# Kernel tuning notes

Measured on AMD Instinct MI355X. Metric: run time of the kernel, lower is better.

## Reference

```python
import jax, jax.numpy as jnp
import numpy as np

# Faithful JAX translation of fastmax_function with mask=True, p=1, normalize=0.
# In that branch the torch code sets temperature = 1 and uses a0 = a1 = 1.

def setup_inputs() -> dict:
    key = jax.random.key(0)
    kq, kk, kv = jax.random.split(key, 3)
    b, h, n, d = 2, 8, 8192, 32
    q = jax.random.normal(kq, (b, h, n, d), dtype=jnp.float32)
    k = jax.random.normal(kk, (b, h, n, d), dtype=jnp.float32)
    v = jax.random.normal(kv, (b, h, n, d), dtype=jnp.float32)
    return {"q": q, "k": k, "v": v}


def reference(q, k, v):
    # q, k, v: (b, h, n, d); causal (mask=True), p=1, a0=a1=1, temperature=1
    b, h, n, d = q.shape
    # first term: running sum of values
    first = jnp.cumsum(v, axis=2)                                  # (b,h,n,d)
    # second term: q_i . (sum_{j<=i} k_j v_j^T)
    kv = jnp.einsum('bhnd,bhne->bhnde', k, v)                      # (b,h,n,d,d)
    kv_cs = jnp.cumsum(kv, axis=2)                                 # (b,h,n,d,d)
    second = jnp.einsum('bhnd,bhnde->bhne', q, kv_cs)              # (b,h,n,d)
    # denominator: i + q_i . (sum_{j<=i} k_j)
    k_cs = jnp.cumsum(k, axis=2)                                   # (b,h,n,d)
    div1 = jnp.arange(1, n + 1, dtype=q.dtype)                     # (n,)
    div2 = jnp.einsum('bhnd,bhnd->bhn', q, k_cs)                   # (b,h,n)
    div = (div1[None, None, :] + div2)[..., None]                  # (b,h,n,1)
    return (first + second) / div
```

## Files before the change

### kernel.cpp

```cpp
#include <hip/hip_runtime.h>


#define D      32
#define C      64
#define NCHUNK 128
#define GSIZE  8
#define NGROUP 16
#define BH     16
#define NBLK   (BH * NCHUNK)
#define STATE  1088

typedef __attribute__((ext_vector_type(8))) short bf16x8;
typedef __attribute__((ext_vector_type(4))) float f32x4;
typedef __attribute__((ext_vector_type(4))) unsigned short u16x4;

__device__ __forceinline__ unsigned short f2bf(float x) {
  union { float f; unsigned u; } c; c.f = x;
  unsigned r = (c.u + 0x7FFFu + ((c.u >> 16) & 1u)) >> 16;
  return (unsigned short)r;
}

__device__ __forceinline__ int permcol(int e) {
  return (e & 1) ? (16 + (e >> 1)) : (e >> 1);
}

__device__ __forceinline__ float4 add4(float4 a, float4 b) {
  return make_float4(a.x + b.x, a.y + b.y, a.z + b.z, a.w + b.w);
}

__global__ __launch_bounds__(256) void state_scan_kernel(
    const float* __restrict__ k, const float* __restrict__ v,
    float* __restrict__ states, float* __restrict__ totals) {
  int blk = blockIdx.x;
  int c0  = blk * GSIZE;
  const float4* kp = (const float4*)k + (size_t)c0 * 512;
  const float4* vp = (const float4*)v + (size_t)c0 * 512;

  __shared__ __align__(16) unsigned short kT[D * 72];
  __shared__ __align__(16) unsigned short vT[D * 72];
  __shared__ __align__(16) float4 psK[256];
  __shared__ __align__(16) float4 psV[256];

  int t  = threadIdx.x;
  int j0 = t >> 3;
  int cb = (t & 7) * 4;
  int lane = t & 63, w = t >> 6;
  int m16 = lane & 15, quad = lane >> 4;
  int mb = w >> 1, nb = w & 1;
  int d1b = 16 * mb + quad * 4;
  int d2  = 16 * nb + m16;

  float pref[4] = {0.f, 0.f, 0.f, 0.f};
  float tailpref = 0.f;

  float4 kA = kp[t], kB = kp[t + 256];
  float4 vA = vp[t], vB = vp[t + 256];

  for (int ci = 0; ci < GSIZE; ++ci) {
    {
      const float* ka = &kA.x; const float* kb = &kB.x;
      const float* va = &vA.x; const float* vb = &vB.x;
#pragma unroll
      for (int cc = 0; cc < 4; ++cc) {
        kT[(cb + cc) * 72 + j0]      = f2bf(ka[cc]);
        kT[(cb + cc) * 72 + j0 + 32] = f2bf(kb[cc]);
        vT[(cb + cc) * 72 + j0]      = f2bf(va[cc]);
        vT[(cb + cc) * 72 + j0 + 32] = f2bf(vb[cc]);
      }
      psK[t] = make_float4(kA.x + kB.x, kA.y + kB.y, kA.z + kB.z, kA.w + kB.w);
      psV[t] = make_float4(vA.x + vB.x, vA.y + vB.y, vA.z + vB.z, vA.w + vB.w);
    }
    __syncthreads();

    if (ci + 1 < GSIZE) {
      const float4* kn = kp + (size_t)(ci + 1) * 512;
      const float4* vn = vp + (size_t)(ci + 1) * 512;
      kA = kn[t]; kB = kn[t + 256];
      vA = vn[t]; vB = vn[t + 256];
    }

    f32x4 acc = {0.f, 0.f, 0.f, 0.f};
#pragma unroll
    for (int kb2 = 0; kb2 < 2; ++kb2) {
      bf16x8 a = *(const bf16x8*)&kT[(16 * mb + m16) * 72 + kb2 * 32 + quad * 8];
      bf16x8 b = *(const bf16x8*)&vT[(16 * nb + m16) * 72 + kb2 * 32 + quad * 8];
      acc = __builtin_amdgcn_mfma_f32_16x16x32_bf16(a, b, acc, 0, 0, 0);
    }
    float csum = 0.f;
    if (t < 64) {
      int ee = t & 31;
      const float* ps = (t < 32) ? (const float*)psK : (const float*)psV;
#pragma unroll
      for (int m = 0; m < 32; ++m) csum += ps[ee + 32 * m];
    }

    float* stC = states + (size_t)(c0 + ci) * STATE;
#pragma unroll
    for (int reg = 0; reg < 4; ++reg) {
      stC[(d1b + reg) * 32 + d2] = pref[reg];
      pref[reg] += acc[reg];
    }
    if (t < 64) {
      stC[1024 + t] = tailpref;
      tailpref += csum;
    }
    __syncthreads();
  }

  float* tp = totals + (size_t)blk * STATE;
#pragma unroll
  for (int reg = 0; reg < 4; ++reg) tp[(d1b + reg) * 32 + d2] = pref[reg];
  if (t < 64) tp[1024 + t] = tailpref;
}

__global__ __launch_bounds__(256) void output_kernel(
    const float* __restrict__ q, const float* __restrict__ k,
    const float* __restrict__ v, const float* __restrict__ states,
    const float* __restrict__ totals, float* __restrict__ out) {
  int blk = blockIdx.x;
  int c   = blk & 127;
  int bh  = blk >> 7;
  int g   = c >> 3;
  size_t off = (size_t)blk * (C * D);
  const float4* qp4 = (const float4*)q + (size_t)blk * 512;
  const float4* kp4 = (const float4*)k + (size_t)blk * 512;
  const float4* vp4 = (const float4*)v + (size_t)blk * 512;
  const float4* st4 = (const float4*)(states + (size_t)blk * STATE);
  const float4* tb4 = (const float4*)(totals + (size_t)(bh * NGROUP) * STATE);

  __shared__ __align__(16) unsigned short qbf[C * 40];
  __shared__ __align__(16) unsigned short kbf[C * 40];
  __shared__ __align__(16) unsigned short vTbf[D * 72];
  __shared__ __align__(16) unsigned short kvTbf[D * 40];
  __shared__ __align__(16) unsigned short Tbf[C * 72];
  __shared__ __align__(16) float q_s[C * 36];
  __shared__ __align__(16) float kc_s[C * 36];
  __shared__ __align__(16) float gtot[8 * 32];
  __shared__ __align__(16) float kpre_s[D], vpre_s[D], invdiv_s[C];

  int t  = threadIdx.x;
  int j0 = t >> 3;
  int cb = (t & 7) * 4;

  float4 qA = qp4[t], qB = qp4[t + 256];
  float4 kA = kp4[t], kB = kp4[t + 256];
  float4 vA = vp4[t], vB = vp4[t + 256];
  float4 sv = st4[t];
  float4 tail = make_float4(0.f, 0.f, 0.f, 0.f);
  if (t < 16) tail = st4[256 + t];

  {
    float4 a0 = make_float4(0.f, 0.f, 0.f, 0.f), a1 = a0, a2 = a0, a3 = a0;
    int gp = 0;
    for (; gp + 4 <= g; gp += 4) {
      a0 = add4(a0, tb4[(size_t)(gp + 0) * 272 + t]);
      a1 = add4(a1, tb4[(size_t)(gp + 1) * 272 + t]);
      a2 = add4(a2, tb4[(size_t)(gp + 2) * 272 + t]);
      a3 = add4(a3, tb4[(size_t)(gp + 3) * 272 + t]);
    }
    for (; gp < g; ++gp) a0 = add4(a0, tb4[(size_t)gp * 272 + t]);
    sv = add4(sv, add4(add4(a0, a1), add4(a2, a3)));
    if (t < 16)
      for (int g2 = 0; g2 < g; ++g2)
        tail = add4(tail, tb4[(size_t)g2 * 272 + 256 + t]);
  }

  for (int z = t; z < (C * 72) / 8; z += 256)
    ((uint4*)Tbf)[z] = make_uint4(0, 0, 0, 0);

  *(float4*)&q_s[j0 * 36 + cb]         = qA;
  *(float4*)&q_s[(j0 + 32) * 36 + cb]  = qB;
  *(float4*)&kc_s[j0 * 36 + cb]        = kA;
  *(float4*)&kc_s[(j0 + 32) * 36 + cb] = kB;
  *(u16x4*)&qbf[j0 * 40 + cb] =
      (u16x4){f2bf(qA.x), f2bf(qA.y), f2bf(qA.z), f2bf(qA.w)};
  *(u16x4*)&qbf[(j0 + 32) * 40 + cb] =
      (u16x4){f2bf(qB.x), f2bf(qB.y), f2bf(qB.z), f2bf(qB.w)};
  *(u16x4*)&kbf[j0 * 40 + cb] =
      (u16x4){f2bf(kA.x), f2bf(kA.y), f2bf(kA.z), f2bf(kA.w)};
  *(u16x4*)&kbf[(j0 + 32) * 40 + cb] =
      (u16x4){f2bf(kB.x), f2bf(kB.y), f2bf(kB.z), f2bf(kB.w)};
  {
    const float* va = &vA.x; const float* vb = &vB.x;
    const float* sp = &sv.x;
#pragma unroll
    for (int cc = 0; cc < 4; ++cc) {
      int n = permcol(cb + cc);
      vTbf[n * 72 + j0]      = f2bf(va[cc]);
      vTbf[n * 72 + j0 + 32] = f2bf(vb[cc]);
      kvTbf[n * 40 + j0]     = f2bf(sp[cc]);
    }
  }
  if (t < 8)            ((float4*)kpre_s)[t]     = tail;
  else if (t < 16)      ((float4*)vpre_s)[t - 8] = tail;
  __syncthreads();

  int lane = t & 63, w = t >> 6;
  int m16 = lane & 15, quad = lane >> 4;

  const bf16x8 aQ = *(const bf16x8*)&qbf[(16 * w + m16) * 40 + quad * 8];
  for (int jb = 0; jb <= w; ++jb) {
    bf16x8 bK = *(const bf16x8*)&kbf[(16 * jb + m16) * 40 + quad * 8];
    f32x4 cS = {0.f, 0.f, 0.f, 0.f};
    cS = __builtin_amdgcn_mfma_f32_16x16x32_bf16(aQ, bK, cS, 0, 0, 0);
    int jcol = 16 * jb + m16;
#pragma unroll
    for (int reg = 0; reg < 4; ++reg) {
      int i = 16 * w + quad * 4 + reg;
      float tv = (jcol <= i) ? (1.f + cS[reg]) : 0.f;
      Tbf[i * 72 + jcol] = f2bf(tv);
    }
  }
  int rg = t >> 5;
  int e  = t & 31;
  float vals[8];
  {
    float run = 0.f;
#pragma unroll
    for (int r = 0; r < 8; ++r) {
      vals[r] = kc_s[(rg * 8 + r) * 36 + e];
      run += vals[r];
    }
    gtot[rg * 32 + e] = run;
  }
  __syncthreads();

  {
    float offv = kpre_s[e];
    for (int g2 = 0; g2 < rg; ++g2) offv += gtot[g2 * 32 + e];
    float cacc = offv;
#pragma unroll
    for (int r = 0; r < 8; ++r) {
      cacc += vals[r];
      kc_s[(rg * 8 + r) * 36 + e] = cacc;
    }
  }
  __syncthreads();

  if (t < 64) {
    int i = t;
    float dp = 0.f;
#pragma unroll
    for (int d4 = 0; d4 < 8; ++d4) {
      float4 qv = *(const float4*)&q_s[i * 36 + 4 * d4];
      float4 kc = *(const float4*)&kc_s[i * 36 + 4 * d4];
      dp += qv.x * kc.x + qv.y * kc.y + qv.z * kc.z + qv.w * kc.w;
    }
    invdiv_s[i] = 1.f / ((float)(c * C + i + 1) + dp);
  }
  f32x4 o0 = {0.f, 0.f, 0.f, 0.f}, o1 = {0.f, 0.f, 0.f, 0.f};
  {
    bf16x8 b0 = *(const bf16x8*)&kvTbf[(m16)      * 40 + quad * 8];
    bf16x8 b1 = *(const bf16x8*)&kvTbf[(16 + m16) * 40 + quad * 8];
    o0 = __builtin_amdgcn_mfma_f32_16x16x32_bf16(aQ, b0, o0, 0, 0, 0);
    o1 = __builtin_amdgcn_mfma_f32_16x16x32_bf16(aQ, b1, o1, 0, 0, 0);
  }
  int kbcnt = (w >= 2) ? 2 : 1;
  for (int kb2 = 0; kb2 < kbcnt; ++kb2) {
    bf16x8 aT = *(const bf16x8*)&Tbf[(16 * w + m16) * 72 + kb2 * 32 + quad * 8];
    bf16x8 b0 = *(const bf16x8*)&vTbf[(m16)      * 72 + kb2 * 32 + quad * 8];
    bf16x8 b1 = *(const bf16x8*)&vTbf[(16 + m16) * 72 + kb2 * 32 + quad * 8];
    o0 = __builtin_amdgcn_mfma_f32_16x16x32_bf16(aT, b0, o0, 0, 0, 0);
    o1 = __builtin_amdgcn_mfma_f32_16x16x32_bf16(aT, b1, o1, 0, 0, 0);
  }
  __syncthreads();

  int e0 = 2 * m16;
#pragma unroll
  for (int reg = 0; reg < 4; ++reg) {
    int i = 16 * w + quad * 4 + reg;
    float id = invdiv_s[i];
    float2 o;
    o.x = (vpre_s[e0]     + o0[reg]) * id;
    o.y = (vpre_s[e0 + 1] + o1[reg]) * id;
    *(float2*)&out[off + (size_t)i * D + e0] = o;
  }
}

extern "C" void kernel_launch(void* const* d_in, const int* in_sizes, int n_in,
                              void* d_out, int out_size, void* d_ws, size_t ws_size,
                              hipStream_t stream) {
  const float* q = (const float*)d_in[0];
  const float* k = (const float*)d_in[1];
  const float* v = (const float*)d_in[2];
  float* out    = (float*)d_out;
  float* states = (float*)d_ws;
  float* totals = states + (size_t)NBLK * STATE;

  state_scan_kernel<<<BH * NGROUP, 256, 0, stream>>>(k, v, states, totals);
  output_kernel<<<NBLK, 256, 0, stream>>>(q, k, v, states, totals, out);
}
```

Measured before the change: 111.0 us.

## Store per-chunk states in bf16 and pre-scan group totals in a separate kernel

Per-chunk prefix states are written as bf16, pre-transposed into the layout the output kernel needs, which roughly halves the state traffic between kernels and replaces scattered shared-memory stores with one vectorized store. A new small kernel turns the group totals into an exclusive prefix in place, so each output block reads one totals row instead of summing up to 15 rows. This adds a third kernel launch and rounds the intra-group prefix to bf16 before the fp32 group offset is added, which can change precision slightly.

```diff
diff --git a/kernel.cpp b/kernel.cpp
--- a/kernel.cpp
+++ b/kernel.cpp
@@ -9,6 +9,7 @@
 #define BH     16
 #define NBLK   (BH * NCHUNK)
 #define STATE  1088
+#define STCH   1152
 
 typedef __attribute__((ext_vector_type(8))) short bf16x8;
 typedef __attribute__((ext_vector_type(4))) float f32x4;
@@ -19,18 +20,20 @@
   unsigned r = (c.u + 0x7FFFu + ((c.u >> 16) & 1u)) >> 16;
   return (unsigned short)r;
 }
-
+__device__ __forceinline__ float bf2f(unsigned short u) {
+  union { unsigned u; float f; } c; c.u = ((unsigned)u) << 16;
+  return c.f;
+}
 __device__ __forceinline__ int permcol(int e) {
   return (e & 1) ? (16 + (e >> 1)) : (e >> 1);
 }
-
 __device__ __forceinline__ float4 add4(float4 a, float4 b) {
   return make_float4(a.x + b.x, a.y + b.y, a.z + b.z, a.w + b.w);
 }
 
 __global__ __launch_bounds__(256) void state_scan_kernel(
     const float* __restrict__ k, const float* __restrict__ v,
-    float* __restrict__ states, float* __restrict__ totals) {
+    unsigned short* __restrict__ states, float* __restrict__ totals) {
   int blk = blockIdx.x;
   int c0  = blk * GSIZE;
   const float4* kp = (const float4*)k + (size_t)c0 * 512;
@@ -49,6 +52,7 @@
   int mb = w >> 1, nb = w & 1;
   int d1b = 16 * mb + quad * 4;
   int d2  = 16 * nb + m16;
+  int n   = permcol(d2);
 
   float pref[4] = {0.f, 0.f, 0.f, 0.f};
   float tailpref = 0.f;
@@ -94,28 +98,41 @@
       for (int m = 0; m < 32; ++m) csum += ps[ee + 32 * m];
     }
 
-    float* stC = states + (size_t)(c0 + ci) * STATE;
-#pragma unroll
-    for (int reg = 0; reg < 4; ++reg) {
-      stC[(d1b + reg) * 32 + d2] = pref[reg];
-      pref[reg] += acc[reg];
-    }
+    unsigned short* stC = states + (size_t)(c0 + ci) * STCH;
+    *(u16x4*)&stC[n * 32 + d1b] =
+        (u16x4){f2bf(pref[0]), f2bf(pref[1]), f2bf(pref[2]), f2bf(pref[3])};
+#pragma unroll
+    for (int reg = 0; reg < 4; ++reg) pref[reg] += acc[reg];
     if (t < 64) {
-      stC[1024 + t] = tailpref;
+      ((float*)(stC + 1024))[t] = tailpref;
       tailpref += csum;
     }
     __syncthreads();
   }
 
   float* tp = totals + (size_t)blk * STATE;
-#pragma unroll
-  for (int reg = 0; reg < 4; ++reg) tp[(d1b + reg) * 32 + d2] = pref[reg];
+  *(float4*)&tp[n * 32 + d1b] =
+      make_float4(pref[0], pref[1], pref[2], pref[3]);
   if (t < 64) tp[1024 + t] = tailpref;
+}
+
+__global__ __launch_bounds__(256) void totals_scan_kernel(float* __restrict__ totals) {
+  int gidx = blockIdx.x * 256 + threadIdx.x;
+  int bh = gidx / STATE;
+  int e  = gidx % STATE;
+  float* base = totals + (size_t)(bh * NGROUP) * STATE + e;
+  float a = 0.f;
+#pragma unroll
+  for (int g = 0; g < NGROUP; ++g) {
+    float s = base[(size_t)g * STATE];
+    base[(size_t)g * STATE] = a;
+    a += s;
+  }
 }
 
 __global__ __launch_bounds__(256) void output_kernel(
     const float* __restrict__ q, const float* __restrict__ k,
-    const float* __restrict__ v, const float* __restrict__ states,
+    const float* __restrict__ v, const unsigned short* __restrict__ states,
     const float* __restrict__ totals, float* __restrict__ out) {
   int blk = blockIdx.x;
   int c   = blk & 127;
@@ -125,8 +142,8 @@
   const float4* qp4 = (const float4*)q + (size_t)blk * 512;
   const float4* kp4 = (const float4*)k + (size_t)blk * 512;
   const float4* vp4 = (const float4*)v + (size_t)blk * 512;
-  const float4* st4 = (const float4*)(states + (size_t)blk * STATE);
-  const float4* tb4 = (const float4*)(totals + (size_t)(bh * NGROUP) * STATE);
+  const unsigned short* stc = states + (size_t)blk * STCH;
+  const float* tb = totals + (size_t)(bh * NGROUP + g) * STATE;
 
   __shared__ __align__(16) unsigned short qbf[C * 40];
   __shared__ __align__(16) unsigned short kbf[C * 40];
@@ -145,25 +162,12 @@
   float4 qA = qp4[t], qB = qp4[t + 256];
   float4 kA = kp4[t], kB = kp4[t + 256];
   float4 vA = vp4[t], vB = vp4[t + 256];
-  float4 sv = st4[t];
+  uint2  su  = *(const uint2*)&stc[t * 4];
+  float4 tv4 = *(const float4*)&tb[t * 4];
   float4 tail = make_float4(0.f, 0.f, 0.f, 0.f);
-  if (t < 16) tail = st4[256 + t];
-
-  {
-    float4 a0 = make_float4(0.f, 0.f, 0.f, 0.f), a1 = a0, a2 = a0, a3 = a0;
-    int gp = 0;
-    for (; gp + 4 <= g; gp += 4) {
-      a0 = add4(a0, tb4[(size_t)(gp + 0) * 272 + t]);
-      a1 = add4(a1, tb4[(size_t)(gp + 1) * 272 + t]);
-      a2 = add4(a2, tb4[(size_t)(gp + 2) * 272 + t]);
-      a3 = add4(a3, tb4[(size_t)(gp + 3) * 272 + t]);
-    }
-    for (; gp < g; ++gp) a0 = add4(a0, tb4[(size_t)gp * 272 + t]);
-    sv = add4(sv, add4(add4(a0, a1), add4(a2, a3)));
-    if (t < 16)
-      for (int g2 = 0; g2 < g; ++g2)
-        tail = add4(tail, tb4[(size_t)g2 * 272 + 256 + t]);
-  }
+  if (t < 16)
+    tail = add4(*(const float4*)((const float*)(stc + 1024) + 4 * t),
+                *(const float4*)&tb[1024 + 4 * t]);
 
   for (int z = t; z < (C * 72) / 8; z += 256)
     ((uint4*)Tbf)[z] = make_uint4(0, 0, 0, 0);
@@ -182,14 +186,20 @@
       (u16x4){f2bf(kB.x), f2bf(kB.y), f2bf(kB.z), f2bf(kB.w)};
   {
     const float* va = &vA.x; const float* vb = &vB.x;
-    const float* sp = &sv.x;
 #pragma unroll
     for (int cc = 0; cc < 4; ++cc) {
       int n = permcol(cb + cc);
       vTbf[n * 72 + j0]      = f2bf(va[cc]);
       vTbf[n * 72 + j0 + 32] = f2bf(vb[cc]);
-      kvTbf[n * 40 + j0]     = f2bf(sp[cc]);
-    }
+    }
+  }
+  {
+    float s0 = bf2f((unsigned short)(su.x & 0xffff)) + tv4.x;
+    float s1 = bf2f((unsigned short)(su.x >> 16))    + tv4.y;
+    float s2 = bf2f((unsigned short)(su.y & 0xffff)) + tv4.z;
+    float s3 = bf2f((unsigned short)(su.y >> 16))    + tv4.w;
+    *(u16x4*)&kvTbf[(t >> 3) * 40 + (t & 7) * 4] =
+        (u16x4){f2bf(s0), f2bf(s1), f2bf(s2), f2bf(s3)};
   }
   if (t < 8)            ((float4*)kpre_s)[t]     = tail;
   else if (t < 16)      ((float4*)vpre_s)[t - 8] = tail;
@@ -283,10 +293,11 @@
   const float* q = (const float*)d_in[0];
   const float* k = (const float*)d_in[1];
   const float* v = (const float*)d_in[2];
-  float* out    = (float*)d_out;
-  float* states = (float*)d_ws;
-  float* totals = states + (size_t)NBLK * STATE;
+  float* out = (float*)d_out;
+  unsigned short* states = (unsigned short*)d_ws;
+  float* totals = (float*)(states + (size_t)NBLK * STCH);
 
   state_scan_kernel<<<BH * NGROUP, 256, 0, stream>>>(k, v, states, totals);
+  totals_scan_kernel<<<(BH * STATE) / 256, 256, 0, stream>>>(totals);
   output_kernel<<<NBLK, 256, 0, stream>>>(q, k, v, states, totals, out);
 }
```

Measured after the change: 103.8 us. 6.5% less time.
